# Kernel tuning notes

Hardware: AMD Instinct MI355X
Metric: run time of the kernel (lower is better)

The kernel has to match this reference:

```python
import jax, jax.numpy as jnp
import numpy as np

N, F, E = 1024, 32, 20


def setup_inputs() -> dict:
    key = jax.random.key(0)
    ks = jax.random.split(key, 18)
    f32 = jnp.float32
    nrm = lambda k, shape, s=1.0: (jax.random.normal(k, shape, f32) * s)
    scalar = nrm(ks[0], (N, 1, F))
    vector = nrm(ks[1], (N, 3, F))
    expansion = nrm(ks[2], (N, N, E))
    d = nrm(ks[3], (N, N, 3))
    direction = d / (jnp.linalg.norm(d, axis=-1, keepdims=True) + 1e-6)
    mask = (jax.random.uniform(ks[4], (N, N, 1)) < 0.9).astype(f32)
    w = 0.1  # weight scale
    return {
        "scalar": scalar, "vector": vector, "expansion": expansion,
        "direction": direction, "mask": mask,
        # message.msg_left: Linear(F,F) -> SiLU -> Linear(F,3F)
        "mL_w1": nrm(ks[5], (F, F), w), "mL_b1": jnp.zeros((F,), f32),
        "mL_w2": nrm(ks[6], (F, 3 * F), w), "mL_b2": jnp.zeros((3 * F,), f32),
        # message.msg_right: Linear(E, 3F)
        "mR_w": nrm(ks[7], (E, 3 * F), w), "mR_b": jnp.zeros((3 * F,), f32),
        # update.upd_right: Linear(2F,F) -> SiLU -> Linear(F,3F)
        "uR_w1": nrm(ks[8], (2 * F, F), w), "uR_b1": jnp.zeros((F,), f32),
        "uR_w2": nrm(ks[9], (F, 3 * F), w), "uR_b2": jnp.zeros((3 * F,), f32),
        # update.U / update.V: Linear(F,F,bias=False)
        "U_w": nrm(ks[10], (F, F), w),
        "V_w": nrm(ks[11], (F, F), w),
    }


def _message(s, v, expansion, direction, mask,
             mL_w1, mL_b1, mL_w2, mL_b2, mR_w, mR_b):
    # msg_left(s): [N,1,F] -> [N,1,3F]
    left = jax.nn.silu(s @ mL_w1 + mL_b1) @ mL_w2 + mL_b2
    # msg_right(expansion): [N,N,E] -> [N,N,3F] -> [N,N,1,3F]
    right = (expansion @ mR_w + mR_b)[..., None, :]
    prod = left * right                      # [N,N,1,3F]
    a, b, c = jnp.split(prod, 3, axis=-1)    # each [N,N,1,F]
    mask_ = mask[..., None]                  # [N,N,1,1]
    delta_s = jnp.sum(mask_ * b, axis=-3)    # [N,1,F]
    dv = v * a + direction[..., None] * c    # [N,N,3,F]
    delta_v = jnp.sum(mask_ * dv, axis=-3)   # [N,3,F]
    return delta_s, delta_v


def _update(scalar, vector, uR_w1, uR_b1, uR_w2, uR_b2, U_w, V_w):
    left = vector @ U_w                      # [N,3,F]
    right = vector @ V_w                     # [N,3,F]
    right_norm = jnp.linalg.norm(right, axis=-2, keepdims=True)   # [N,1,F]
    feats = jnp.concatenate((scalar, right_norm), axis=-1)        # [N,1,2F]
    feats = jax.nn.silu(feats @ uR_w1 + uR_b1) @ uR_w2 + uR_b2    # [N,1,3F]
    a, b, c = jnp.split(feats, 3, axis=-1)
    delta_v = a * left                                            # [N,3,F]
    inner = jnp.sum(left * right, axis=-2, keepdims=True)         # [N,1,F]
    delta_s = inner * b + c
    return delta_s, delta_v


def reference(scalar, vector, expansion, direction, mask,
              mL_w1, mL_b1, mL_w2, mL_b2, mR_w, mR_b,
              uR_w1, uR_b1, uR_w2, uR_b2, U_w, V_w):
    ds, dv = _message(scalar, vector, expansion, direction, mask,
                      mL_w1, mL_b1, mL_w2, mL_b2, mR_w, mR_b)
    scalar = scalar + ds
    vector = vector + dv
    ds, dv = _update(scalar, vector, uR_w1, uR_b1, uR_w2, uR_b2, U_w, V_w)
    return scalar + ds, vector + dv
```

## Files before the change

kernel.cpp:

```cpp
#include <hip/hip_runtime.h>
#include <hip/hip_bf16.h>
#include <math.h>

#define NN 1024
#define JS 256
#define NSL 4
#define PB 72
#define LP 40

typedef __attribute__((ext_vector_type(8))) short v8s;
typedef __attribute__((ext_vector_type(4))) float v4f;

#define MFMA(a, b, c) __builtin_amdgcn_mfma_f32_16x16x32_bf16((a), (b), (c), 0, 0, 0)

#define BAR() asm volatile("s_waitcnt lgkmcnt(0)\n\ts_barrier" ::: "memory")

static __device__ __forceinline__ float silu_f(float x) {
    return x / (1.0f + __expf(-x));
}
static __device__ __forceinline__ unsigned short f2bf(float x) {
    __hip_bfloat16 h = __float2bfloat16(x);
    unsigned short u; __builtin_memcpy(&u, &h, 2); return u;
}
static __device__ __forceinline__ unsigned pack2bf(float lo, float hi) {
    __hip_bfloat162 h = __float22bfloat162_rn(make_float2(lo, hi));
    unsigned u; __builtin_memcpy(&u, &h, 4); return u;
}

extern "C" __global__ __launch_bounds__(128)
void node_kernel(const float* __restrict__ scalar,
                 const float* __restrict__ vector,
                 const float* __restrict__ mL_w1, const float* __restrict__ mL_b1,
                 const float* __restrict__ mL_w2, const float* __restrict__ mL_b2,
                 unsigned short* __restrict__ RT)
{
    const int j = blockIdx.x;
    const int t = threadIdx.x;
    __shared__ float ss[32], sh[32], sleft[96];

    if (t < 32) ss[t] = scalar[j * 32 + t];
    __syncthreads();
    if (t < 32) {
        float a = mL_b1[t];
        #pragma unroll
        for (int k = 0; k < 32; k++) a = fmaf(ss[k], mL_w1[k * 32 + t], a);
        sh[t] = silu_f(a);
    }
    __syncthreads();
    if (t < 96) {
        float a = mL_b2[t];
        #pragma unroll
        for (int k = 0; k < 32; k++) a = fmaf(sh[k], mL_w2[k * 96 + t], a);
        sleft[t] = a;
    }
    __syncthreads();
    for (int n = t; n < 160; n += 128) {
        float val;
        if (n < 32)        val = sleft[32 + n];
        else if (n < 128)  val = vector[j * 96 + (n - 32)] * sleft[(n - 32) & 31];
        else               val = sleft[64 + (n - 128)];
        RT[(size_t)n * NN + j] = f2bf(val);
    }
}

extern "C" __global__ __launch_bounds__(256, 4)
void edge_mfma_kernel(const float* __restrict__ expansion,
                      const float* __restrict__ direction,
                      const float* __restrict__ mask,
                      const float* __restrict__ mR_w, const float* __restrict__ mR_b,
                      const unsigned short* __restrict__ RT,
                      float* __restrict__ part)
{
    const int t = threadIdx.x;
    const int wave = t >> 6;
    const int lane = t & 63;
    const int lrow = lane & 15;
    const int quad = lane >> 4;
    const int jp = lane >> 2;
    const int g  = lane & 3;
    const int jl = jp * 2;

    const int bx = blockIdx.x;
    const int slice = bx & (NSL - 1);
    const int j0 = slice * JS;
    const int i = (bx >> 2) * 2 + (wave >> 1);

    __shared__ __align__(16) unsigned short BSm[160 * PB];
    __shared__ __align__(16) char Wm[13824];

    for (int u = t; u < 160 * 8; u += 256) {
        const int row = u >> 3, seg = u & 7;
        *(uint4*)(BSm + row * PB + seg * 8) =
            *(const uint4*)(RT + (size_t)row * NN + j0 + seg * 8);
    }
    BAR();

    if ((wave & 1) == 0) {
        unsigned short* L1 = (unsigned short*)(Wm + (wave >> 1) * 6912);
        float* S = (float*)((char*)BSm + (wave >> 1) * 5472);

        v4f acc[16];
        #pragma unroll
        for (int q = 0; q < 16; ++q) acc[q] = (v4f){0.f, 0.f, 0.f, 0.f};

        float4 fa, fb; float cea, ceb, m0, m1;
        {
            const size_t jg = (size_t)i * NN + j0 + jl;
            fa = *(const float4*)(expansion + jg * 20 + 4 * g);
            fb = *(const float4*)(expansion + (jg + 1) * 20 + 4 * g);
            cea = expansion[jg * 20 + 16 + g];
            ceb = expansion[(jg + 1) * 20 + 16 + g];
            const float2 mm = *(const float2*)(mask + jg);
            m0 = mm.x; m1 = mm.y;
        }

        for (int ss2 = 0; ss2 < 4; ++ss2) {
            #pragma unroll
            for (int ch = 0; ch < 2; ++ch) {
                {
                    const float ea[4] = {fa.x, fa.y, fa.z, fa.w};
                    const float eb[4] = {fb.x, fb.y, fb.z, fb.w};
                    #pragma unroll
                    for (int k = 0; k < 4; ++k)
                        *(unsigned*)(L1 + (4 * g + k) * LP + jl) =
                            pack2bf(m0 * ea[k], m1 * eb[k]);
                    *(unsigned*)(L1 + (16 + g) * LP + jl) = pack2bf(m0 * cea, m1 * ceb);
                    if (g == 0) *(unsigned*)(L1 + 20 * LP + jl) = pack2bf(m0, m1);
                }
                {
                    const int u = ss2 * 2 + ch;
                    const int un = (u < 7) ? u + 1 : 7;
                    const size_t jg = (size_t)i * NN + j0 + un * 32 + jl;
                    fa = *(const float4*)(expansion + jg * 20 + 4 * g);
                    fb = *(const float4*)(expansion + (jg + 1) * 20 + 4 * g);
                    cea = expansion[jg * 20 + 16 + g];
                    ceb = expansion[(jg + 1) * 20 + 16 + g];
                    const float2 mm = *(const float2*)(mask + jg);
                    m0 = mm.x; m1 = mm.y;
                }
                {
                    const int ko = quad * 8;
                    const int kl = ch * 32 + ko;
                    const v8s a0 = *(const v8s*)(L1 + lrow * LP + ko);
                    const v8s a1 = *(const v8s*)(L1 + (16 + lrow) * LP + ko);
                    #pragma unroll
                    for (int nt = 0; nt < 8; ++nt) {
                        const v8s b = *(const v8s*)(BSm + (nt * 16 + lrow) * PB + kl);
                        acc[nt]     = MFMA(a0, b, acc[nt]);
                        acc[8 + nt] = MFMA(a1, b, acc[8 + nt]);
                    }
                }
            }
            BAR();
            if (ss2 < 3) {
                for (int u2 = t; u2 < 160 * 8; u2 += 256) {
                    const int row = u2 >> 3, seg = u2 & 7;
                    *(uint4*)(BSm + row * PB + seg * 8) =
                        *(const uint4*)(RT + (size_t)row * NN + j0 + (ss2 + 1) * 64 + seg * 8);
                }
                BAR();
            }
        }

        float* pdst = part + ((size_t)i * NSL + slice) * 224;
        #pragma unroll
        for (int h = 0; h < 2; ++h) {
            #pragma unroll
            for (int mt = 0; mt < 2; ++mt)
            #pragma unroll
            for (int q = 0; q < 4; ++q)
            #pragma unroll
            for (int r = 0; r < 4; ++r) {
                const int row = mt * 16 + quad * 4 + r;
                if (row <= 20) S[row * 65 + q * 16 + lrow] = acc[mt * 8 + h * 4 + q][r];
            }
            const int col = h * 64 + lane;
            const int fw = (col < 32) ? (32 + col) : ((col - 32) & 31);
            float v = mR_b[fw] * S[20 * 65 + lane];
            #pragma unroll
            for (int e = 0; e < 20; ++e)
                v = fmaf(mR_w[e * 96 + fw], S[e * 65 + lane], v);
            pdst[col] = v;
        }
    } else {
        unsigned short* L2 = (unsigned short*)(Wm + 1792 + (wave >> 1) * 6912);
        float* S = (float*)((char*)BSm + 10944 + (wave >> 1) * 4288);

        v4f acc[8];
        #pragma unroll
        for (int q = 0; q < 8; ++q) acc[q] = (v4f){0.f, 0.f, 0.f, 0.f};

        float4 fa, fb;
        float cea, ceb, m0, m1, da0, da1, da2, db0, db1, db2;
        {
            const size_t jg = (size_t)i * NN + j0 + jl;
            fa = *(const float4*)(expansion + jg * 20 + 4 * g);
            fb = *(const float4*)(expansion + (jg + 1) * 20 + 4 * g);
            cea = expansion[jg * 20 + 16 + g];
            ceb = expansion[(jg + 1) * 20 + 16 + g];
            const float2 mm = *(const float2*)(mask + jg);
            m0 = mm.x; m1 = mm.y;
            const float2 dd0 = *(const float2*)(direction + jg * 3);
            const float2 dd1 = *(const float2*)(direction + jg * 3 + 2);
            const float2 dd2 = *(const float2*)(direction + jg * 3 + 4);
            da0 = dd0.x; da1 = dd0.y; da2 = dd1.x;
            db0 = dd1.y; db1 = dd2.x; db2 = dd2.y;
        }

        for (int ss2 = 0; ss2 < 4; ++ss2) {
            #pragma unroll
            for (int ch = 0; ch < 2; ++ch) {
                {
                    const float pa[3] = {m0 * da0, m0 * da1, m0 * da2};
                    const float pb[3] = {m1 * db0, m1 * db1, m1 * db2};
                    const float ea[4] = {fa.x, fa.y, fa.z, fa.w};
                    const float eb[4] = {fb.x, fb.y, fb.z, fb.w};
                    #pragma unroll
                    for (int d = 0; d < 3; ++d) {
                        #pragma unroll
                        for (int k = 0; k < 4; ++k)
                            *(unsigned*)(L2 + (d * 20 + 4 * g + k) * LP + jl) =
                                pack2bf(pa[d] * ea[k], pb[d] * eb[k]);
                        *(unsigned*)(L2 + (d * 20 + 16 + g) * LP + jl) =
                            pack2bf(pa[d] * cea, pb[d] * ceb);
                    }
                    if (g == 0) {
                        *(unsigned*)(L2 + (60 + 0) * LP + jl) = pack2bf(pa[0], pb[0]);
                        *(unsigned*)(L2 + (60 + 1) * LP + jl) = pack2bf(pa[1], pb[1]);
                        *(unsigned*)(L2 + (60 + 2) * LP + jl) = pack2bf(pa[2], pb[2]);
                    }
                }
                {
                    const int u = ss2 * 2 + ch;
                    const int un = (u < 7) ? u + 1 : 7;
                    const size_t jg = (size_t)i * NN + j0 + un * 32 + jl;
                    fa = *(const float4*)(expansion + jg * 20 + 4 * g);
                    fb = *(const float4*)(expansion + (jg + 1) * 20 + 4 * g);
                    cea = expansion[jg * 20 + 16 + g];
                    ceb = expansion[(jg + 1) * 20 + 16 + g];
                    const float2 mm = *(const float2*)(mask + jg);
                    m0 = mm.x; m1 = mm.y;
                    const float2 dd0 = *(const float2*)(direction + jg * 3);
                    const float2 dd1 = *(const float2*)(direction + jg * 3 + 2);
                    const float2 dd2 = *(const float2*)(direction + jg * 3 + 4);
                    da0 = dd0.x; da1 = dd0.y; da2 = dd1.x;
                    db0 = dd1.y; db1 = dd2.x; db2 = dd2.y;
                }
                {
                    const int ko = quad * 8;
                    const int kl = ch * 32 + ko;
                    const v8s c0 = *(const v8s*)(L2 + (lrow) * LP + ko);
                    const v8s c1 = *(const v8s*)(L2 + (16 + lrow) * LP + ko);
                    const v8s c2 = *(const v8s*)(L2 + (32 + lrow) * LP + ko);
                    const v8s c3 = *(const v8s*)(L2 + (48 + lrow) * LP + ko);
                    const v8s b0 = *(const v8s*)(BSm + (128 + lrow) * PB + kl);
                    const v8s b1 = *(const v8s*)(BSm + (144 + lrow) * PB + kl);
                    acc[0] = MFMA(c0, b0, acc[0]); acc[1] = MFMA(c0, b1, acc[1]);
                    acc[2] = MFMA(c1, b0, acc[2]); acc[3] = MFMA(c1, b1, acc[3]);
                    acc[4] = MFMA(c2, b0, acc[4]); acc[5] = MFMA(c2, b1, acc[5]);
                    acc[6] = MFMA(c3, b0, acc[6]); acc[7] = MFMA(c3, b1, acc[7]);
                }
            }
            BAR();
            if (ss2 < 3) {
                for (int u2 = t; u2 < 160 * 8; u2 += 256) {
                    const int row = u2 >> 3, seg = u2 & 7;
                    *(uint4*)(BSm + row * PB + seg * 8) =
                        *(const uint4*)(RT + (size_t)row * NN + j0 + (ss2 + 1) * 64 + seg * 8);
                }
                BAR();
            }
        }

        float* pdst = part + ((size_t)i * NSL + slice) * 224;
        #pragma unroll
        for (int h2 = 0; h2 < 2; ++h2) {
            #pragma unroll
            for (int mt = 0; mt < 4; ++mt)
            #pragma unroll
            for (int r = 0; r < 4; ++r) {
                const int row = mt * 16 + quad * 4 + r;
                if (row <= 62) S[row * 17 + lrow] = acc[mt * 2 + h2][r];
            }
            if (lane < 48) {
                const int dd = lane >> 4, f16 = lane & 15;
                const int f = h2 * 16 + f16;
                float v = mR_b[64 + f] * S[(60 + dd) * 17 + f16];
                #pragma unroll
                for (int e = 0; e < 20; ++e)
                    v = fmaf(mR_w[e * 96 + 64 + f], S[(dd * 20 + e) * 17 + f16], v);
                pdst[128 + dd * 32 + f] = v;
            }
        }
    }
}

extern "C" __global__ __launch_bounds__(256)
void combine_kernel(const float* __restrict__ scalar,
                    const float* __restrict__ vector,
                    const float* __restrict__ uR_w1, const float* __restrict__ uR_b1,
                    const float* __restrict__ uR_w2, const float* __restrict__ uR_b2,
                    const float* __restrict__ U_w,  const float* __restrict__ V_w,
                    const float* __restrict__ part,
                    float* __restrict__ out)
{
    const int i = blockIdx.x;
    const int t = threadIdx.x;
    __shared__ float pcomb[224];
    __shared__ float snew[32], vnew[96];
    __shared__ float lU[96], rV[96], rnorm[32], h2[32], f2[96];

    if (t < 224) {
        const float* p = part + (size_t)i * NSL * 224 + t;
        float a = 0.f;
        #pragma unroll
        for (int s = 0; s < NSL; ++s) a += p[s * 224];
        pcomb[t] = a;
    }
    __syncthreads();

    if (t < 128) {
        const int d = t >> 5, ff = t & 31;
        if (d == 0) snew[ff] = scalar[i * 32 + ff] + pcomb[ff];
        else {
            const int q = t - 32;
            vnew[q] = vector[i * 96 + q] + pcomb[32 + q] + pcomb[128 + q];
        }
    }
    __syncthreads();

    if (t < 96) {
        const int d = t >> 5, ff = t & 31;
        float a = 0.0f;
        #pragma unroll
        for (int k = 0; k < 32; k++) a = fmaf(vnew[d * 32 + k], U_w[k * 32 + ff], a);
        lU[t] = a;
    } else if (t >= 128 && t < 224) {
        const int dt = t - 128, d = dt >> 5, ff = dt & 31;
        float a = 0.0f;
        #pragma unroll
        for (int k = 0; k < 32; k++) a = fmaf(vnew[d * 32 + k], V_w[k * 32 + ff], a);
        rV[dt] = a;
    }
    __syncthreads();
    if (t < 32) {
        const float a = rV[t] * rV[t] + rV[32 + t] * rV[32 + t] + rV[64 + t] * rV[64 + t];
        rnorm[t] = sqrtf(a);
    }
    __syncthreads();
    if (t < 32) {
        float a = uR_b1[t];
        #pragma unroll
        for (int k = 0; k < 32; k++) a = fmaf(snew[k],  uR_w1[k * 32 + t], a);
        #pragma unroll
        for (int k = 0; k < 32; k++) a = fmaf(rnorm[k], uR_w1[(32 + k) * 32 + t], a);
        h2[t] = silu_f(a);
    }
    __syncthreads();
    if (t < 96) {
        float a = uR_b2[t];
        #pragma unroll
        for (int k = 0; k < 32; k++) a = fmaf(h2[k], uR_w2[k * 96 + t], a);
        f2[t] = a;
    }
    __syncthreads();
    if (t < 32) {
        const float inner = lU[t] * rV[t] + lU[32 + t] * rV[32 + t] + lU[64 + t] * rV[64 + t];
        out[i * 32 + t] = snew[t] + inner * f2[32 + t] + f2[64 + t];
    } else if (t >= 64 && t < 160) {
        const int dt = t - 64, ff = dt & 31;
        out[32768 + i * 96 + dt] = vnew[dt] + f2[ff] * lU[dt];
    }
}

extern "C" void kernel_launch(void* const* d_in, const int* in_sizes, int n_in,
                              void* d_out, int out_size, void* d_ws, size_t ws_size,
                              hipStream_t stream) {
    const float* scalar    = (const float*)d_in[0];
    const float* vector    = (const float*)d_in[1];
    const float* expansion = (const float*)d_in[2];
    const float* direction = (const float*)d_in[3];
    const float* mask      = (const float*)d_in[4];
    const float* mL_w1     = (const float*)d_in[5];
    const float* mL_b1     = (const float*)d_in[6];
    const float* mL_w2     = (const float*)d_in[7];
    const float* mL_b2     = (const float*)d_in[8];
    const float* mR_w      = (const float*)d_in[9];
    const float* mR_b      = (const float*)d_in[10];
    const float* uR_w1     = (const float*)d_in[11];
    const float* uR_b1     = (const float*)d_in[12];
    const float* uR_w2     = (const float*)d_in[13];
    const float* uR_b2     = (const float*)d_in[14];
    const float* U_w       = (const float*)d_in[15];
    const float* V_w       = (const float*)d_in[16];
    float* out = (float*)d_out;

    unsigned short* RT = (unsigned short*)d_ws;
    float* part = (float*)((char*)d_ws + 160 * NN * 2);

    hipLaunchKernelGGL(node_kernel, dim3(NN), dim3(128), 0, stream,
                       scalar, vector, mL_w1, mL_b1, mL_w2, mL_b2, RT);
    hipLaunchKernelGGL(edge_mfma_kernel, dim3(2048), dim3(256), 0, stream,
                       expansion, direction, mask, mR_w, mR_b, RT, part);
    hipLaunchKernelGGL(combine_kernel, dim3(NN), dim3(256), 0, stream,
                       scalar, vector, uR_w1, uR_b1, uR_w2, uR_b2, U_w, V_w,
                       part, out);
}
```

Measured before the change: 195.0 us.

## Load RT tiles via global_load_lds with XOR swizzle, stage mask in LDS, deepen prefetch

```diff
diff --git a/kernel.cpp b/kernel.cpp
--- a/kernel.cpp
+++ b/kernel.cpp
@@ -5,7 +5,6 @@
 #define NN 1024
 #define JS 256
 #define NSL 4
-#define PB 72
 #define LP 40
 
 typedef __attribute__((ext_vector_type(8))) short v8s;
@@ -14,6 +13,13 @@
 #define MFMA(a, b, c) __builtin_amdgcn_mfma_f32_16x16x32_bf16((a), (b), (c), 0, 0, 0)
 
 #define BAR() asm volatile("s_waitcnt lgkmcnt(0)\n\ts_barrier" ::: "memory")
+#define VM0() asm volatile("s_waitcnt vmcnt(0)" ::: "memory")
+
+static __device__ __forceinline__ void gll16(const void* g, void* l) {
+    __builtin_amdgcn_global_load_lds(
+        (const __attribute__((address_space(1))) unsigned int*)g,
+        (__attribute__((address_space(3))) unsigned int*)l, 16, 0, 0);
+}
 
 static __device__ __forceinline__ float silu_f(float x) {
     return x / (1.0f + __expf(-x));
@@ -59,7 +65,8 @@
         if (n < 32)        val = sleft[32 + n];
         else if (n < 128)  val = vector[j * 96 + (n - 32)] * sleft[(n - 32) & 31];
         else               val = sleft[64 + (n - 128)];
-        RT[(size_t)n * NN + j] = f2bf(val);
+        const int jsw = j ^ ((n & 7) << 3);
+        RT[(size_t)n * NN + jsw] = f2bf(val);
     }
 }
 
@@ -83,84 +90,91 @@
     const int bx = blockIdx.x;
     const int slice = bx & (NSL - 1);
     const int j0 = slice * JS;
-    const int i = (bx >> 2) * 2 + (wave >> 1);
-
-    __shared__ __align__(16) unsigned short BSm[160 * PB];
+    const int iw = wave >> 1;
+    const int i = (bx >> 2) * 2 + iw;
+
+    __shared__ __align__(16) unsigned short BSm[160 * 64];
     __shared__ __align__(16) char Wm[13824];
-
-    for (int u = t; u < 160 * 8; u += 256) {
-        const int row = u >> 3, seg = u & 7;
-        *(uint4*)(BSm + row * PB + seg * 8) =
-            *(const uint4*)(RT + (size_t)row * NN + j0 + seg * 8);
-    }
+    __shared__ __align__(16) float mLds[2 * JS];
+
+    const unsigned short* rtbase = RT + ((size_t)(t >> 3) * NN) + ((t & 7) * 8);
+    unsigned short* lds_dst = BSm + t * 8;
+
+    #pragma unroll
+    for (int k = 0; k < 5; ++k)
+        gll16(rtbase + (size_t)k * 32 * NN + j0, lds_dst + k * 2048);
+    for (int q = t; q < 2 * JS; q += 256)
+        mLds[q] = mask[(size_t)((bx >> 2) * 2 + (q >> 8)) * NN + j0 + (q & 255)];
+    VM0();
     BAR();
 
+    const int kswz = (lrow & 7) << 3;
+    const int ko = quad * 8;
+
     if ((wave & 1) == 0) {
-        unsigned short* L1 = (unsigned short*)(Wm + (wave >> 1) * 6912);
-        float* S = (float*)((char*)BSm + (wave >> 1) * 5472);
+        unsigned short* L1 = (unsigned short*)(Wm + iw * 6912);
+        float* S = (float*)((char*)BSm + iw * 5472);
 
         v4f acc[16];
         #pragma unroll
         for (int q = 0; q < 16; ++q) acc[q] = (v4f){0.f, 0.f, 0.f, 0.f};
 
-        float4 fa, fb; float cea, ceb, m0, m1;
-        {
-            const size_t jg = (size_t)i * NN + j0 + jl;
-            fa = *(const float4*)(expansion + jg * 20 + 4 * g);
-            fb = *(const float4*)(expansion + (jg + 1) * 20 + 4 * g);
-            cea = expansion[jg * 20 + 16 + g];
-            ceb = expansion[(jg + 1) * 20 + 16 + g];
-            const float2 mm = *(const float2*)(mask + jg);
-            m0 = mm.x; m1 = mm.y;
-        }
+        const float* expA = expansion + ((size_t)i * NN + j0 + jl) * 20;
+
+        float4 faA = *(const float4*)(expA + 4 * g);
+        float4 fbA = *(const float4*)(expA + 20 + 4 * g);
+        float4 faB = *(const float4*)(expA + 640 + 4 * g);
+        float4 fbB = *(const float4*)(expA + 660 + 4 * g);
+        float cea = expA[16 + g], ceb = expA[36 + g];
+        float2 mc = *(const float2*)(&mLds[iw * JS + jl]);
+
+#define T1_CHUNK(CU, CH, fa_c, fb_c)                                          \
+  {                                                                            \
+    {                                                                \
+      const float ea[4] = {fa_c.x, fa_c.y, fa_c.z, fa_c.w};                    \
+      const float eb[4] = {fb_c.x, fb_c.y, fb_c.z, fb_c.w};                    \
+      _Pragma("unroll")                                                        \
+      for (int k = 0; k < 4; ++k)                                              \
+        *(unsigned*)(L1 + (4 * g + k) * LP + jl) =                             \
+            pack2bf(mc.x * ea[k], mc.y * eb[k]);                               \
+      *(unsigned*)(L1 + (16 + g) * LP + jl) = pack2bf(mc.x * cea, mc.y * ceb); \
+      if (g == 0) *(unsigned*)(L1 + 20 * LP + jl) = pack2bf(mc.x, mc.y);       \
+    }                                                                          \
+    {                               \
+      const int n2 = ((CU) + 2 < 8) ? (CU) + 2 : 7;                            \
+      const int n1 = ((CU) + 1 < 8) ? (CU) + 1 : 7;                            \
+      fa_c = *(const float4*)(expA + n2 * 640 + 4 * g);                        \
+      fb_c = *(const float4*)(expA + n2 * 640 + 20 + 4 * g);                   \
+      cea = expA[n1 * 640 + 16 + g];  ceb = expA[n1 * 640 + 36 + g];           \
+      mc = *(const float2*)(&mLds[iw * JS + n1 * 32 + jl]);                    \
+    }                                                                          \
+    {                                         \
+      const v8s a0 = *(const v8s*)(L1 + lrow * LP + ko);                       \
+      const v8s a1 = *(const v8s*)(L1 + (16 + lrow) * LP + ko);                \
+      const int klz = ((CH) * 32 + ko) ^ kswz;                                 \
+      _Pragma("unroll")                                                        \
+      for (int nt = 0; nt < 8; ++nt) {                                         \
+        const v8s b = *(const v8s*)(BSm + (nt * 16 + lrow) * 64 + klz);        \
+        acc[nt]     = MFMA(a0, b, acc[nt]);                                    \
+        acc[8 + nt] = MFMA(a1, b, acc[8 + nt]);                                \
+      }                                                                        \
+    }                                                                          \
+  }
 
         for (int ss2 = 0; ss2 < 4; ++ss2) {
-            #pragma unroll
-            for (int ch = 0; ch < 2; ++ch) {
-                {
-                    const float ea[4] = {fa.x, fa.y, fa.z, fa.w};
-                    const float eb[4] = {fb.x, fb.y, fb.z, fb.w};
-                    #pragma unroll
-                    for (int k = 0; k < 4; ++k)
-                        *(unsigned*)(L1 + (4 * g + k) * LP + jl) =
-                            pack2bf(m0 * ea[k], m1 * eb[k]);
-                    *(unsigned*)(L1 + (16 + g) * LP + jl) = pack2bf(m0 * cea, m1 * ceb);
-                    if (g == 0) *(unsigned*)(L1 + 20 * LP + jl) = pack2bf(m0, m1);
-                }
-                {
-                    const int u = ss2 * 2 + ch;
-                    const int un = (u < 7) ? u + 1 : 7;
-                    const size_t jg = (size_t)i * NN + j0 + un * 32 + jl;
-                    fa = *(const float4*)(expansion + jg * 20 + 4 * g);
-                    fb = *(const float4*)(expansion + (jg + 1) * 20 + 4 * g);
-                    cea = expansion[jg * 20 + 16 + g];
-                    ceb = expansion[(jg + 1) * 20 + 16 + g];
-                    const float2 mm = *(const float2*)(mask + jg);
-                    m0 = mm.x; m1 = mm.y;
-                }
-                {
-                    const int ko = quad * 8;
-                    const int kl = ch * 32 + ko;
-                    const v8s a0 = *(const v8s*)(L1 + lrow * LP + ko);
-                    const v8s a1 = *(const v8s*)(L1 + (16 + lrow) * LP + ko);
-                    #pragma unroll
-                    for (int nt = 0; nt < 8; ++nt) {
-                        const v8s b = *(const v8s*)(BSm + (nt * 16 + lrow) * PB + kl);
-                        acc[nt]     = MFMA(a0, b, acc[nt]);
-                        acc[8 + nt] = MFMA(a1, b, acc[8 + nt]);
-                    }
-                }
-            }
+            T1_CHUNK(2 * ss2,     0, faA, fbA);
+            T1_CHUNK(2 * ss2 + 1, 1, faB, fbB);
             BAR();
             if (ss2 < 3) {
-                for (int u2 = t; u2 < 160 * 8; u2 += 256) {
-                    const int row = u2 >> 3, seg = u2 & 7;
-                    *(uint4*)(BSm + row * PB + seg * 8) =
-                        *(const uint4*)(RT + (size_t)row * NN + j0 + (ss2 + 1) * 64 + seg * 8);
-                }
+                const unsigned short* src = rtbase + j0 + (ss2 + 1) * 64;
+                #pragma unroll
+                for (int k = 0; k < 5; ++k)
+                    gll16(src + (size_t)k * 32 * NN, lds_dst + k * 2048);
+                VM0();
                 BAR();
             }
         }
+#undef T1_CHUNK
 
         float* pdst = part + ((size_t)i * NSL + slice) * 224;
         #pragma unroll
@@ -183,94 +197,88 @@
             pdst[col] = v;
         }
     } else {
-        unsigned short* L2 = (unsigned short*)(Wm + 1792 + (wave >> 1) * 6912);
-        float* S = (float*)((char*)BSm + 10944 + (wave >> 1) * 4288);
+        unsigned short* L2 = (unsigned short*)(Wm + 1792 + iw * 6912);
+        float* S = (float*)((char*)BSm + 10944 + iw * 4288);
 
         v4f acc[8];
         #pragma unroll
         for (int q = 0; q < 8; ++q) acc[q] = (v4f){0.f, 0.f, 0.f, 0.f};
 
-        float4 fa, fb;
-        float cea, ceb, m0, m1, da0, da1, da2, db0, db1, db2;
-        {
-            const size_t jg = (size_t)i * NN + j0 + jl;
-            fa = *(const float4*)(expansion + jg * 20 + 4 * g);
-            fb = *(const float4*)(expansion + (jg + 1) * 20 + 4 * g);
-            cea = expansion[jg * 20 + 16 + g];
-            ceb = expansion[(jg + 1) * 20 + 16 + g];
-            const float2 mm = *(const float2*)(mask + jg);
-            m0 = mm.x; m1 = mm.y;
-            const float2 dd0 = *(const float2*)(direction + jg * 3);
-            const float2 dd1 = *(const float2*)(direction + jg * 3 + 2);
-            const float2 dd2 = *(const float2*)(direction + jg * 3 + 4);
-            da0 = dd0.x; da1 = dd0.y; da2 = dd1.x;
-            db0 = dd1.y; db1 = dd2.x; db2 = dd2.y;
-        }
+        const float* expA = expansion + ((size_t)i * NN + j0 + jl) * 20;
+        const float* dirA = direction + ((size_t)i * NN + j0 + jl) * 3;
+
+        float4 faA = *(const float4*)(expA + 4 * g);
+        float4 fbA = *(const float4*)(expA + 20 + 4 * g);
+        float4 faB = *(const float4*)(expA + 640 + 4 * g);
+        float4 fbB = *(const float4*)(expA + 660 + 4 * g);
+        float cea = expA[16 + g], ceb = expA[36 + g];
+        float2 mc = *(const float2*)(&mLds[iw * JS + jl]);
+        float2 dv0 = *(const float2*)(dirA);
+        float2 dv1 = *(const float2*)(dirA + 2);
+        float2 dv2 = *(const float2*)(dirA + 4);
+
+#define T2_CHUNK(CU, CH, fa_c, fb_c)                                           \
+  {                                                                             \
+    {                                                                 \
+      const float pa[3] = {mc.x * dv0.x, mc.x * dv0.y, mc.x * dv1.x};           \
+      const float pb[3] = {mc.y * dv1.y, mc.y * dv2.x, mc.y * dv2.y};           \
+      const float ea[4] = {fa_c.x, fa_c.y, fa_c.z, fa_c.w};                     \
+      const float eb[4] = {fb_c.x, fb_c.y, fb_c.z, fb_c.w};                     \
+      _Pragma("unroll")                                                         \
+      for (int d = 0; d < 3; ++d) {                                             \
+        _Pragma("unroll")                                                       \
+        for (int k = 0; k < 4; ++k)                                             \
+          *(unsigned*)(L2 + (d * 20 + 4 * g + k) * LP + jl) =                   \
+              pack2bf(pa[d] * ea[k], pb[d] * eb[k]);                            \
+        *(unsigned*)(L2 + (d * 20 + 16 + g) * LP + jl) =                        \
+            pack2bf(pa[d] * cea, pb[d] * ceb);                                  \
+      }                                                                         \
+      if (g == 0) {                                                             \
+        *(unsigned*)(L2 + (60 + 0) * LP + jl) = pack2bf(pa[0], pb[0]);          \
+        *(unsigned*)(L2 + (60 + 1) * LP + jl) = pack2bf(pa[1], pb[1]);          \
+        *(unsigned*)(L2 + (60 + 2) * LP + jl) = pack2bf(pa[2], pb[2]);          \
+      }                                                                         \
+    }                                                                           \
+    {                            \
+      const int n2 = ((CU) + 2 < 8) ? (CU) + 2 : 7;                             \
+      const int n1 = ((CU) + 1 < 8) ? (CU) + 1 : 7;                             \
+      fa_c = *(const float4*)(expA + n2 * 640 + 4 * g);                         \
+      fb_c = *(const float4*)(expA + n2 * 640 + 20 + 4 * g);                    \
+      cea = expA[n1 * 640 + 16 + g];  ceb = expA[n1 * 640 + 36 + g];            \
+      dv0 = *(const float2*)(dirA + n1 * 96);                                   \
+      dv1 = *(const float2*)(dirA + n1 * 96 + 2);                               \
+      dv2 = *(const float2*)(dirA + n1 * 96 + 4);                               \
+      mc = *(const float2*)(&mLds[iw * JS + n1 * 32 + jl]);                     \
+    }                                                                           \
+    {                                          \
+      const v8s c0 = *(const v8s*)(L2 + (lrow) * LP + ko);                      \
+      const v8s c1 = *(const v8s*)(L2 + (16 + lrow) * LP + ko);                 \
+      const v8s c2 = *(const v8s*)(L2 + (32 + lrow) * LP + ko);                 \
+      const v8s c3 = *(const v8s*)(L2 + (48 + lrow) * LP + ko);                 \
+      const int klz = ((CH) * 32 + ko) ^ kswz;                                  \
+      const v8s b0 = *(const v8s*)(BSm + (128 + lrow) * 64 + klz);              \
+      const v8s b1 = *(const v8s*)(BSm + (144 + lrow) * 64 + klz);              \
+      acc[0] = MFMA(c0, b0, acc[0]); acc[1] = MFMA(c0, b1, acc[1]);             \
+      acc[2] = MFMA(c1, b0, acc[2]); acc[3] = MFMA(c1, b1, acc[3]);             \
+      acc[4] = MFMA(c2, b0, acc[4]); acc[5] = MFMA(c2, b1, acc[5]);             \
+      acc[6] = MFMA(c3, b0, acc[6]); acc[7] = MFMA(c3, b1, acc[7]);             \
+    }                                                                           \
+  }
 
         for (int ss2 = 0; ss2 < 4; ++ss2) {
-            #pragma unroll
-            for (int ch = 0; ch < 2; ++ch) {
-                {
-                    const float pa[3] = {m0 * da0, m0 * da1, m0 * da2};
-                    const float pb[3] = {m1 * db0, m1 * db1, m1 * db2};
-                    const float ea[4] = {fa.x, fa.y, fa.z, fa.w};
-                    const float eb[4] = {fb.x, fb.y, fb.z, fb.w};
-                    #pragma unroll
-                    for (int d = 0; d < 3; ++d) {
-                        #pragma unroll
-                        for (int k = 0; k < 4; ++k)
-                            *(unsigned*)(L2 + (d * 20 + 4 * g + k) * LP + jl) =
-                                pack2bf(pa[d] * ea[k], pb[d] * eb[k]);
-                        *(unsigned*)(L2 + (d * 20 + 16 + g) * LP + jl) =
-                            pack2bf(pa[d] * cea, pb[d] * ceb);
-                    }
-                    if (g == 0) {
-                        *(unsigned*)(L2 + (60 + 0) * LP + jl) = pack2bf(pa[0], pb[0]);
-                        *(unsigned*)(L2 + (60 + 1) * LP + jl) = pack2bf(pa[1], pb[1]);
-                        *(unsigned*)(L2 + (60 + 2) * LP + jl) = pack2bf(pa[2], pb[2]);
-                    }
-                }
-                {
-                    const int u = ss2 * 2 + ch;
-                    const int un = (u < 7) ? u + 1 : 7;
-                    const size_t jg = (size_t)i * NN + j0 + un * 32 + jl;
-                    fa = *(const float4*)(expansion + jg * 20 + 4 * g);
-                    fb = *(const float4*)(expansion + (jg + 1) * 20 + 4 * g);
-                    cea = expansion[jg * 20 + 16 + g];
-                    ceb = expansion[(jg + 1) * 20 + 16 + g];
-                    const float2 mm = *(const float2*)(mask + jg);
-                    m0 = mm.x; m1 = mm.y;
-                    const float2 dd0 = *(const float2*)(direction + jg * 3);
-                    const float2 dd1 = *(const float2*)(direction + jg * 3 + 2);
-                    const float2 dd2 = *(const float2*)(direction + jg * 3 + 4);
-                    da0 = dd0.x; da1 = dd0.y; da2 = dd1.x;
-                    db0 = dd1.y; db1 = dd2.x; db2 = dd2.y;
-                }
-                {
-                    const int ko = quad * 8;
-                    const int kl = ch * 32 + ko;
-                    const v8s c0 = *(const v8s*)(L2 + (lrow) * LP + ko);
-                    const v8s c1 = *(const v8s*)(L2 + (16 + lrow) * LP + ko);
-                    const v8s c2 = *(const v8s*)(L2 + (32 + lrow) * LP + ko);
-                    const v8s c3 = *(const v8s*)(L2 + (48 + lrow) * LP + ko);
-                    const v8s b0 = *(const v8s*)(BSm + (128 + lrow) * PB + kl);
-                    const v8s b1 = *(const v8s*)(BSm + (144 + lrow) * PB + kl);
-                    acc[0] = MFMA(c0, b0, acc[0]); acc[1] = MFMA(c0, b1, acc[1]);
-                    acc[2] = MFMA(c1, b0, acc[2]); acc[3] = MFMA(c1, b1, acc[3]);
-                    acc[4] = MFMA(c2, b0, acc[4]); acc[5] = MFMA(c2, b1, acc[5]);
-                    acc[6] = MFMA(c3, b0, acc[6]); acc[7] = MFMA(c3, b1, acc[7]);
-                }
-            }
+            T2_CHUNK(2 * ss2,     0, faA, fbA);
+            T2_CHUNK(2 * ss2 + 1, 1, faB, fbB);
             BAR();
             if (ss2 < 3) {
-                for (int u2 = t; u2 < 160 * 8; u2 += 256) {
-                    const int row = u2 >> 3, seg = u2 & 7;
-                    *(uint4*)(BSm + row * PB + seg * 8) =
-                        *(const uint4*)(RT + (size_t)row * NN + j0 + (ss2 + 1) * 64 + seg * 8);
-                }
+                const unsigned short* src = rtbase + j0 + (ss2 + 1) * 64;
+                #pragma unroll
+                for (int k = 0; k < 5; ++k)
+                    gll16(src + (size_t)k * 32 * NN, lds_dst + k * 2048);
+                VM0();
                 BAR();
             }
         }
+#undef T2_CHUNK
 
         float* pdst = part + ((size_t)i * NSL + slice) * 224;
         #pragma unroll
```

New measurement: 221.0 us. 1.13x slower.

## Load RT tiles with direct global-to-LDS loads and XOR-swizzled layout

Applied to the files above, without the earlier changes.

```diff
diff --git a/kernel.cpp b/kernel.cpp
--- a/kernel.cpp
+++ b/kernel.cpp
@@ -5,7 +5,6 @@
 #define NN 1024
 #define JS 256
 #define NSL 4
-#define PB 72
 #define LP 40
 
 typedef __attribute__((ext_vector_type(8))) short v8s;
@@ -14,6 +13,13 @@
 #define MFMA(a, b, c) __builtin_amdgcn_mfma_f32_16x16x32_bf16((a), (b), (c), 0, 0, 0)
 
 #define BAR() asm volatile("s_waitcnt lgkmcnt(0)\n\ts_barrier" ::: "memory")
+#define VM0() asm volatile("s_waitcnt vmcnt(0)" ::: "memory")
+
+static __device__ __forceinline__ void gll16(const void* g, void* l) {
+    __builtin_amdgcn_global_load_lds(
+        (const __attribute__((address_space(1))) unsigned int*)g,
+        (__attribute__((address_space(3))) unsigned int*)l, 16, 0, 0);
+}
 
 static __device__ __forceinline__ float silu_f(float x) {
     return x / (1.0f + __expf(-x));
@@ -59,7 +65,8 @@
         if (n < 32)        val = sleft[32 + n];
         else if (n < 128)  val = vector[j * 96 + (n - 32)] * sleft[(n - 32) & 31];
         else               val = sleft[64 + (n - 128)];
-        RT[(size_t)n * NN + j] = f2bf(val);
+        const int jsw = j ^ ((n & 7) << 3);
+        RT[(size_t)n * NN + jsw] = f2bf(val);
     }
 }
 
@@ -83,36 +90,41 @@
     const int bx = blockIdx.x;
     const int slice = bx & (NSL - 1);
     const int j0 = slice * JS;
-    const int i = (bx >> 2) * 2 + (wave >> 1);
-
-    __shared__ __align__(16) unsigned short BSm[160 * PB];
+    const int iw = wave >> 1;
+    const int i = (bx >> 2) * 2 + iw;
+
+    __shared__ __align__(16) unsigned short BSm[160 * 64];
     __shared__ __align__(16) char Wm[13824];
-
-    for (int u = t; u < 160 * 8; u += 256) {
-        const int row = u >> 3, seg = u & 7;
-        *(uint4*)(BSm + row * PB + seg * 8) =
-            *(const uint4*)(RT + (size_t)row * NN + j0 + seg * 8);
-    }
+    __shared__ __align__(16) float mLds[2 * JS];
+
+    const unsigned short* rtbase = RT + ((size_t)(t >> 3) * NN) + ((t & 7) * 8) + j0;
+    unsigned short* lds_dst = BSm + t * 8;
+
+    #pragma unroll
+    for (int k = 0; k < 5; ++k)
+        gll16(rtbase + (size_t)k * 32 * NN, lds_dst + k * 2048);
+    for (int q = t; q < 2 * JS; q += 256)
+        mLds[q] = mask[(size_t)((bx >> 2) * 2 + (q >> 8)) * NN + j0 + (q & 255)];
+    VM0();
     BAR();
 
+    const int kswz = (lrow & 7) << 3;
+    const int ko = quad * 8;
+
     if ((wave & 1) == 0) {
-        unsigned short* L1 = (unsigned short*)(Wm + (wave >> 1) * 6912);
-        float* S = (float*)((char*)BSm + (wave >> 1) * 5472);
+        unsigned short* L1 = (unsigned short*)(Wm + iw * 6912);
+        float* S = (float*)((char*)BSm + iw * 5472);
 
         v4f acc[16];
         #pragma unroll
         for (int q = 0; q < 16; ++q) acc[q] = (v4f){0.f, 0.f, 0.f, 0.f};
 
-        float4 fa, fb; float cea, ceb, m0, m1;
-        {
-            const size_t jg = (size_t)i * NN + j0 + jl;
-            fa = *(const float4*)(expansion + jg * 20 + 4 * g);
-            fb = *(const float4*)(expansion + (jg + 1) * 20 + 4 * g);
-            cea = expansion[jg * 20 + 16 + g];
-            ceb = expansion[(jg + 1) * 20 + 16 + g];
-            const float2 mm = *(const float2*)(mask + jg);
-            m0 = mm.x; m1 = mm.y;
-        }
+        const float* expA = expansion + ((size_t)i * NN + j0 + jl) * 20;
+
+        float4 fa = *(const float4*)(expA + 4 * g);
+        float4 fb = *(const float4*)(expA + 20 + 4 * g);
+        float cea = expA[16 + g], ceb = expA[36 + g];
+        float2 mc = *(const float2*)(&mLds[iw * JS + jl]);
 
         for (int ss2 = 0; ss2 < 4; ++ss2) {
             #pragma unroll
@@ -123,29 +135,26 @@
                     #pragma unroll
                     for (int k = 0; k < 4; ++k)
                         *(unsigned*)(L1 + (4 * g + k) * LP + jl) =
-                            pack2bf(m0 * ea[k], m1 * eb[k]);
-                    *(unsigned*)(L1 + (16 + g) * LP + jl) = pack2bf(m0 * cea, m1 * ceb);
-                    if (g == 0) *(unsigned*)(L1 + 20 * LP + jl) = pack2bf(m0, m1);
+                            pack2bf(mc.x * ea[k], mc.y * eb[k]);
+                    *(unsigned*)(L1 + (16 + g) * LP + jl) = pack2bf(mc.x * cea, mc.y * ceb);
+                    if (g == 0) *(unsigned*)(L1 + 20 * LP + jl) = pack2bf(mc.x, mc.y);
                 }
                 {
                     const int u = ss2 * 2 + ch;
                     const int un = (u < 7) ? u + 1 : 7;
-                    const size_t jg = (size_t)i * NN + j0 + un * 32 + jl;
-                    fa = *(const float4*)(expansion + jg * 20 + 4 * g);
-                    fb = *(const float4*)(expansion + (jg + 1) * 20 + 4 * g);
-                    cea = expansion[jg * 20 + 16 + g];
-                    ceb = expansion[(jg + 1) * 20 + 16 + g];
-                    const float2 mm = *(const float2*)(mask + jg);
-                    m0 = mm.x; m1 = mm.y;
-                }
-                {
-                    const int ko = quad * 8;
-                    const int kl = ch * 32 + ko;
+                    fa = *(const float4*)(expA + un * 640 + 4 * g);
+                    fb = *(const float4*)(expA + un * 640 + 20 + 4 * g);
+                    cea = expA[un * 640 + 16 + g];
+                    ceb = expA[un * 640 + 36 + g];
+                    mc = *(const float2*)(&mLds[iw * JS + un * 32 + jl]);
+                }
+                {
                     const v8s a0 = *(const v8s*)(L1 + lrow * LP + ko);
                     const v8s a1 = *(const v8s*)(L1 + (16 + lrow) * LP + ko);
+                    const int klz = (ch * 32 + ko) ^ kswz;
                     #pragma unroll
                     for (int nt = 0; nt < 8; ++nt) {
-                        const v8s b = *(const v8s*)(BSm + (nt * 16 + lrow) * PB + kl);
+                        const v8s b = *(const v8s*)(BSm + (nt * 16 + lrow) * 64 + klz);
                         acc[nt]     = MFMA(a0, b, acc[nt]);
                         acc[8 + nt] = MFMA(a1, b, acc[8 + nt]);
                     }
@@ -153,11 +162,11 @@
             }
             BAR();
             if (ss2 < 3) {
-                for (int u2 = t; u2 < 160 * 8; u2 += 256) {
-                    const int row = u2 >> 3, seg = u2 & 7;
-                    *(uint4*)(BSm + row * PB + seg * 8) =
-                        *(const uint4*)(RT + (size_t)row * NN + j0 + (ss2 + 1) * 64 + seg * 8);
-                }
+                const unsigned short* src = rtbase + (ss2 + 1) * 64;
+                #pragma unroll
+                for (int k = 0; k < 5; ++k)
+                    gll16(src + (size_t)k * 32 * NN, lds_dst + k * 2048);
+                VM0();
                 BAR();
             }
         }
@@ -183,36 +192,30 @@
             pdst[col] = v;
         }
     } else {
-        unsigned short* L2 = (unsigned short*)(Wm + 1792 + (wave >> 1) * 6912);
-        float* S = (float*)((char*)BSm + 10944 + (wave >> 1) * 4288);
+        unsigned short* L2 = (unsigned short*)(Wm + 1792 + iw * 6912);
+        float* S = (float*)((char*)BSm + 10944 + iw * 4288);
 
         v4f acc[8];
         #pragma unroll
         for (int q = 0; q < 8; ++q) acc[q] = (v4f){0.f, 0.f, 0.f, 0.f};
 
-        float4 fa, fb;
-        float cea, ceb, m0, m1, da0, da1, da2, db0, db1, db2;
-        {
-            const size_t jg = (size_t)i * NN + j0 + jl;
-            fa = *(const float4*)(expansion + jg * 20 + 4 * g);
-            fb = *(const float4*)(expansion + (jg + 1) * 20 + 4 * g);
-            cea = expansion[jg * 20 + 16 + g];
-            ceb = expansion[(jg + 1) * 20 + 16 + g];
-            const float2 mm = *(const float2*)(mask + jg);
-            m0 = mm.x; m1 = mm.y;
-            const float2 dd0 = *(const float2*)(direction + jg * 3);
-            const float2 dd1 = *(const float2*)(direction + jg * 3 + 2);
-            const float2 dd2 = *(const float2*)(direction + jg * 3 + 4);
-            da0 = dd0.x; da1 = dd0.y; da2 = dd1.x;
-            db0 = dd1.y; db1 = dd2.x; db2 = dd2.y;
-        }
+        const float* expA = expansion + ((size_t)i * NN + j0 + jl) * 20;
+        const float* dirA = direction + ((size_t)i * NN + j0 + jl) * 3;
+
+        float4 fa = *(const float4*)(expA + 4 * g);
+        float4 fb = *(const float4*)(expA + 20 + 4 * g);
+        float cea = expA[16 + g], ceb = expA[36 + g];
+        float2 mc = *(const float2*)(&mLds[iw * JS + jl]);
+        float2 dv0 = *(const float2*)(dirA);
+        float2 dv1 = *(const float2*)(dirA + 2);
+        float2 dv2 = *(const float2*)(dirA + 4);
 
         for (int ss2 = 0; ss2 < 4; ++ss2) {
             #pragma unroll
             for (int ch = 0; ch < 2; ++ch) {
                 {
-                    const float pa[3] = {m0 * da0, m0 * da1, m0 * da2};
-                    const float pb[3] = {m1 * db0, m1 * db1, m1 * db2};
+                    const float pa[3] = {mc.x * dv0.x, mc.x * dv0.y, mc.x * dv1.x};
+                    const float pb[3] = {mc.y * dv1.y, mc.y * dv2.x, mc.y * dv2.y};
                     const float ea[4] = {fa.x, fa.y, fa.z, fa.w};
                     const float eb[4] = {fb.x, fb.y, fb.z, fb.w};
                     #pragma unroll
@@ -233,28 +236,23 @@
                 {
                     const int u = ss2 * 2 + ch;
                     const int un = (u < 7) ? u + 1 : 7;
-                    const size_t jg = (size_t)i * NN + j0 + un * 32 + jl;
-                    fa = *(const float4*)(expansion + jg * 20 + 4 * g);
-                    fb = *(const float4*)(expansion + (jg + 1) * 20 + 4 * g);
-                    cea = expansion[jg * 20 + 16 + g];
-                    ceb = expansion[(jg + 1) * 20 + 16 + g];
-                    const float2 mm = *(const float2*)(mask + jg);
-                    m0 = mm.x; m1 = mm.y;
-                    const float2 dd0 = *(const float2*)(direction + jg * 3);
-                    const float2 dd1 = *(const float2*)(direction + jg * 3 + 2);
-                    const float2 dd2 = *(const float2*)(direction + jg * 3 + 4);
-                    da0 = dd0.x; da1 = dd0.y; da2 = dd1.x;
-                    db0 = dd1.y; db1 = dd2.x; db2 = dd2.y;
-                }
-                {
-                    const int ko = quad * 8;
-                    const int kl = ch * 32 + ko;
+                    fa = *(const float4*)(expA + un * 640 + 4 * g);
+                    fb = *(const float4*)(expA + un * 640 + 20 + 4 * g);
+                    cea = expA[un * 640 + 16 + g];
+                    ceb = expA[un * 640 + 36 + g];
+                    dv0 = *(const float2*)(dirA + un * 96);
+                    dv1 = *(const float2*)(dirA + un * 96 + 2);
+                    dv2 = *(const float2*)(dirA + un * 96 + 4);
+                    mc = *(const float2*)(&mLds[iw * JS + un * 32 + jl]);
+                }
+                {
                     const v8s c0 = *(const v8s*)(L2 + (lrow) * LP + ko);
                     const v8s c1 = *(const v8s*)(L2 + (16 + lrow) * LP + ko);
                     const v8s c2 = *(const v8s*)(L2 + (32 + lrow) * LP + ko);
                     const v8s c3 = *(const v8s*)(L2 + (48 + lrow) * LP + ko);
-                    const v8s b0 = *(const v8s*)(BSm + (128 + lrow) * PB + kl);
-                    const v8s b1 = *(const v8s*)(BSm + (144 + lrow) * PB + kl);
+                    const int klz = (ch * 32 + ko) ^ kswz;
+                    const v8s b0 = *(const v8s*)(BSm + (128 + lrow) * 64 + klz);
+                    const v8s b1 = *(const v8s*)(BSm + (144 + lrow) * 64 + klz);
                     acc[0] = MFMA(c0, b0, acc[0]); acc[1] = MFMA(c0, b1, acc[1]);
                     acc[2] = MFMA(c1, b0, acc[2]); acc[3] = MFMA(c1, b1, acc[3]);
                     acc[4] = MFMA(c2, b0, acc[4]); acc[5] = MFMA(c2, b1, acc[5]);
@@ -263,11 +261,11 @@
             }
             BAR();
             if (ss2 < 3) {
-                for (int u2 = t; u2 < 160 * 8; u2 += 256) {
-                    const int row = u2 >> 3, seg = u2 & 7;
-                    *(uint4*)(BSm + row * PB + seg * 8) =
-                        *(const uint4*)(RT + (size_t)row * NN + j0 + (ss2 + 1) * 64 + seg * 8);
-                }
+                const unsigned short* src = rtbase + (ss2 + 1) * 64;
+                #pragma unroll
+                for (int k = 0; k < 5; ++k)
+                    gll16(src + (size_t)k * 32 * NN, lds_dst + k * 2048);
+                VM0();
                 BAR();
             }
         }
```

After: 187.4 us. -3.9%, faster.
